# Optimization experiments

Hardware: AMD Instinct MI355X
Metric: run time of the kernel (lower is better)

The kernel has to match this reference:

```python
import jax, jax.numpy as jnp
import numpy as np

EPS = 1e-6

def _rmsnorm(x, w):
    # x: [..., Dh]
    inv = jax.lax.rsqrt(jnp.mean(x * x, axis=-1, keepdims=True) + EPS)
    return x * inv * w

def _apply_rope(x, rope):
    # x: [B, H, L, Dh], rope: [L, Dh//2, 2]
    L = x.shape[-2]
    cos = rope[:L, :, 0]  # [L, Dh//2]
    sin = rope[:L, :, 1]
    x_even = x[..., 0::2]
    x_odd = x[..., 1::2]
    rot = jnp.stack([x_even * cos - x_odd * sin,
                     x_even * sin + x_odd * cos], axis=-1)  # [B,H,L,Dh//2,2]
    return rot.reshape(*x.shape[:-1], -1)


def setup_inputs() -> dict:
    key = jax.random.key(0)
    ks = jax.random.split(key, 4)
    B, L, D = 2, 2048, 1024
    H, Dh = 16, 64
    x = jax.random.normal(ks[0], (B, L, D), dtype=jnp.float32)
    rope = jax.random.normal(ks[1], (L, Dh // 2, 2), dtype=jnp.float32)
    w_qkv = jax.random.normal(ks[2], (3 * D, D), dtype=jnp.float32) * (1.0 / np.sqrt(D))
    w_proj = jax.random.normal(ks[3], (D, D), dtype=jnp.float32) * (1.0 / np.sqrt(D))
    q_norm_w = jnp.ones((Dh,), dtype=jnp.float32)
    k_norm_w = jnp.ones((Dh,), dtype=jnp.float32)
    return {"x": x, "rope": rope, "w_qkv": w_qkv, "w_proj": w_proj,
            "q_norm_w": q_norm_w, "k_norm_w": k_norm_w}


def reference(x, rope, w_qkv, w_proj, q_norm_w, k_norm_w):
    B, L, D = x.shape
    H = 16
    Dh = D // H
    qkv = jnp.einsum('bld,ed->ble', x, w_qkv).reshape(B, L, 3, H, Dh)
    qkv = jnp.transpose(qkv, (2, 0, 3, 1, 4))  # [3, B, H, L, Dh]
    q, k, v = qkv[0], qkv[1], qkv[2]
    q = _rmsnorm(q, q_norm_w)
    k = _rmsnorm(k, k_norm_w)
    q = _apply_rope(q, rope)
    k = _apply_rope(k, rope)
    scale = 1.0 / np.sqrt(Dh)
    scores = jnp.einsum('bhqd,bhkd->bhqk', q, k) * scale
    attn = jax.nn.softmax(scores, axis=-1)
    out = jnp.einsum('bhqk,bhkd->bhqd', attn, v)  # [B,H,L,Dh]
    out = jnp.transpose(out, (0, 2, 1, 3)).reshape(B, L, D)
    return jnp.einsum('bld,ed->ble', out, w_proj)
```

## Files before the change

kernel.cpp:

```cpp
#include <hip/hip_runtime.h>

typedef unsigned short u16;
typedef unsigned int u32;
typedef __bf16 bf16x8 __attribute__((ext_vector_type(8)));
typedef float f32x4 __attribute__((ext_vector_type(4)));

#define L_SEQ 2048
#define NH 16
#define DH 64
#define D_MODEL 1024
#define ATT_SHIFT2 14.426950408889634f

__device__ __forceinline__ u16 f2bf(float f) {
  union { float f; u32 u; } v; v.f = f;
  u32 u = v.u;
  return (u16)((u + 0x7fffu + ((u >> 16) & 1u)) >> 16);
}
__device__ __forceinline__ float bf2f(u16 b) {
  union { u32 u; float f; } v; v.u = ((u32)b) << 16;
  return v.f;
}
__device__ __forceinline__ u32 pk2(float lo_val, float hi_val) {
  union { float f; u32 u; } a, b;
  a.f = hi_val; b.f = lo_val;
  return __builtin_amdgcn_perm(a.u + 0x8000u, b.u + 0x8000u, 0x07060302u);
}
__device__ __forceinline__ bf16x8 ld8(const u16* p) {
  union { uint4 u; bf16x8 b; } v;
  v.u = *(const uint4*)p;
  return v.b;
}
__device__ __forceinline__ f32x4 fzero4() { f32x4 z = {0.f, 0.f, 0.f, 0.f}; return z; }

__device__ __forceinline__ float fexp2(float x) {
#if __has_builtin(__builtin_amdgcn_exp2f)
  return __builtin_amdgcn_exp2f(x);
#else
  return __expf(x * 0.6931471805599453f);
#endif
}

__device__ __forceinline__ void gll16(const u16* g, u16* l) {
  __builtin_amdgcn_global_load_lds((const __attribute__((address_space(1))) u32*)g,
                                   (__attribute__((address_space(3))) u32*)l, 16, 0, 0);
}

__global__ __launch_bounds__(256) void cvt_bf16(const float* __restrict__ src,
                                                u16* __restrict__ dst, int n4) {
  int i = blockIdx.x * 256 + threadIdx.x;
  if (i >= n4) return;
  float4 v = ((const float4*)src)[i];
  ushort4 o = make_ushort4(f2bf(v.x), f2bf(v.y), f2bf(v.z), f2bf(v.w));
  ((ushort4*)dst)[i] = o;
}

template <int BM, bool OUT_BF16>
__global__ __launch_bounds__(256) void gemm_bt(const u16* __restrict__ A,
                                               const u16* __restrict__ B,
                                               void* __restrict__ Cp,
                                               int N, int K) {
  constexpr int MI = BM / 32;
  __shared__ u16 As[BM * 64];
  __shared__ u16 Bs[128 * 64];
  const int t = threadIdx.x;
  const int lane = t & 63, wv = t >> 6;
  const int col = lane & 15, quad = lane >> 4;
  const int wr = wv >> 1, wc = wv & 1;
  const int m0 = blockIdx.y * BM, n0 = blockIdx.x * 128;

  f32x4 acc[MI][4];
#pragma unroll
  for (int i = 0; i < MI; ++i)
#pragma unroll
    for (int j = 0; j < 4; ++j) acc[i][j] = fzero4();

  for (int kt = 0; kt < K; kt += 64) {
    __syncthreads();
#pragma unroll
    for (int it = 0; it < BM / 32; ++it) {
      int id0 = it * 256 + wv * 64;
      int id = id0 + lane;
      int row = id >> 3, cs = id & 7;
      int csrc = cs ^ (row & 7);
      gll16(A + (size_t)(m0 + row) * K + kt + csrc * 8, As + (size_t)id0 * 8);
    }
#pragma unroll
    for (int it = 0; it < 4; ++it) {
      int id0 = it * 256 + wv * 64;
      int id = id0 + lane;
      int row = id >> 3, cs = id & 7;
      int csrc = cs ^ (row & 7);
      gll16(B + (size_t)(n0 + row) * K + kt + csrc * 8, Bs + (size_t)id0 * 8);
    }
    __syncthreads();
#pragma unroll
    for (int c = 0; c < 2; ++c) {
      bf16x8 af[MI], bfv[4];
#pragma unroll
      for (int f = 0; f < MI; ++f) {
        int r = wr * (BM / 2) + f * 16 + col;
        af[f] = ld8(&As[(r * 8 + ((c * 4 + quad) ^ (r & 7))) * 8]);
      }
#pragma unroll
      for (int f = 0; f < 4; ++f) {
        int rb = wc * 64 + f * 16 + col;
        bfv[f] = ld8(&Bs[(rb * 8 + ((c * 4 + quad) ^ (rb & 7))) * 8]);
      }
#pragma unroll
      for (int i = 0; i < MI; ++i)
#pragma unroll
        for (int j = 0; j < 4; ++j)
          acc[i][j] = __builtin_amdgcn_mfma_f32_16x16x32_bf16(af[i], bfv[j], acc[i][j], 0, 0, 0);
    }
  }
#pragma unroll
  for (int i = 0; i < MI; ++i) {
    int gr = m0 + wr * (BM / 2) + i * 16 + quad * 4;
#pragma unroll
    for (int j = 0; j < 4; ++j) {
      int gc = n0 + wc * 64 + j * 16 + col;
#pragma unroll
      for (int r = 0; r < 4; ++r) {
        if (OUT_BF16)
          ((u16*)Cp)[(size_t)(gr + r) * N + gc] = f2bf(acc[i][j][r]);
        else
          ((float*)Cp)[(size_t)(gr + r) * N + gc] = acc[i][j][r];
      }
    }
  }
}

__global__ __launch_bounds__(256) void qk_norm_rope(const u16* __restrict__ qkvb,
                                                    const float* __restrict__ rope,
                                                    const float* __restrict__ qw,
                                                    const float* __restrict__ kw,
                                                    u16* __restrict__ qb,
                                                    u16* __restrict__ kb) {
  const int t = threadIdx.x;
  const int lane = t & 63, wv = t >> 6;
  const int gid = blockIdx.x * 4 + wv;
  const int l = gid & (L_SEQ - 1);
  const int b = gid >> 11;
  const int lg = lane & 7;
  const u16* base = qkvb + (size_t)gid * 3072 + lane * 8;
  const float QSCALE = 0.125f * 1.4426950408889634f;

  float wqv[8], wkv[8], rp[8];
  {
    float4 a = *(const float4*)(qw + lg * 8);
    float4 c = *(const float4*)(qw + lg * 8 + 4);
    wqv[0]=a.x; wqv[1]=a.y; wqv[2]=a.z; wqv[3]=a.w; wqv[4]=c.x; wqv[5]=c.y; wqv[6]=c.z; wqv[7]=c.w;
    a = *(const float4*)(kw + lg * 8);
    c = *(const float4*)(kw + lg * 8 + 4);
    wkv[0]=a.x; wkv[1]=a.y; wkv[2]=a.z; wkv[3]=a.w; wkv[4]=c.x; wkv[5]=c.y; wkv[6]=c.z; wkv[7]=c.w;
    a = *(const float4*)(rope + (size_t)l * 64 + lg * 8);
    c = *(const float4*)(rope + (size_t)l * 64 + lg * 8 + 4);
    rp[0]=a.x; rp[1]=a.y; rp[2]=a.z; rp[3]=a.w; rp[4]=c.x; rp[5]=c.y; rp[6]=c.z; rp[7]=c.w;
  }

#pragma unroll
  for (int i = 0; i < 2; ++i) {
    bf16x8 q8 = ld8(base + i * 512);
    bf16x8 k8 = ld8(base + 1024 + i * 512);
    float q[8], k[8];
#pragma unroll
    for (int j = 0; j < 8; ++j) { q[j] = (float)q8[j]; k[j] = (float)k8[j]; }
    float sq = 0.f, sk = 0.f;
#pragma unroll
    for (int j = 0; j < 8; ++j) { sq += q[j] * q[j]; sk += k[j] * k[j]; }
    sq += __shfl_xor(sq, 1); sq += __shfl_xor(sq, 2); sq += __shfl_xor(sq, 4);
    sk += __shfl_xor(sk, 1); sk += __shfl_xor(sk, 2); sk += __shfl_xor(sk, 4);
    float qi = rsqrtf(sq * (1.f / 64.f) + 1e-6f);
    float ki = rsqrtf(sk * (1.f / 64.f) + 1e-6f);

    float rq[8], rk[8];
#pragma unroll
    for (int j = 0; j < 4; ++j) {
      float cs = rp[2 * j], sn = rp[2 * j + 1];
      float qe = q[2 * j] * qi * wqv[2 * j], qo = q[2 * j + 1] * qi * wqv[2 * j + 1];
      float ke = k[2 * j] * ki * wkv[2 * j], ko = k[2 * j + 1] * ki * wkv[2 * j + 1];
      rq[2 * j]     = (qe * cs - qo * sn) * QSCALE;
      rq[2 * j + 1] = (qe * sn + qo * cs) * QSCALE;
      rk[2 * j]     = ke * cs - ko * sn;
      rk[2 * j + 1] = ke * sn + ko * cs;
    }
    uint4 qp = make_uint4(pk2(rq[0], rq[1]), pk2(rq[2], rq[3]), pk2(rq[4], rq[5]), pk2(rq[6], rq[7]));
    uint4 kp = make_uint4(pk2(rk[0], rk[1]), pk2(rk[2], rk[3]), pk2(rk[4], rk[5]), pk2(rk[6], rk[7]));
    const int head = (lane >> 3) + i * 8;
    size_t oi = (((size_t)(b * NH + head) * L_SEQ + l) * DH) + lg * 8;
    *(uint4*)(qb + oi) = qp;
    *(uint4*)(kb + oi) = kp;
  }
}

__global__ __launch_bounds__(256) void v_transpose(const u16* __restrict__ qkvb,
                                                   u16* __restrict__ vtb) {
  __shared__ u16 ldsT[64 * 64];
  const int t = threadIdx.x;
  const int bid = blockIdx.x;
  const int bh = bid >> 5;
  const int lt = (bid & 31) * 64;
  const int b = bh >> 4, h = bh & 15;
  const u16* src = qkvb + (size_t)(b * L_SEQ + lt) * 3072 + 2048 + h * 64;
#pragma unroll
  for (int i = 0; i < 2; ++i) {
    int idx = i * 256 + t;
    int ll = idx >> 3, dc = idx & 7;
    uint4 v = *(const uint4*)(src + (size_t)ll * 3072 + dc * 8);
    union { uint4 u; u16 s[8]; } vv; vv.u = v;
#pragma unroll
    for (int j = 0; j < 8; ++j) {
      int dh = dc * 8 + j;
      ldsT[dh * 64 + ((((ll >> 3) ^ (dh >> 3)) & 7) * 8 + (ll & 7))] = vv.s[j];
    }
  }
  __syncthreads();
#pragma unroll
  for (int i = 0; i < 2; ++i) {
    int idx = i * 256 + t;
    int dh = idx >> 3, lc = idx & 7;
    uint4 v = *(const uint4*)&ldsT[dh * 64 + (((lc ^ (dh >> 3)) & 7) * 8)];
    *(uint4*)(vtb + ((size_t)bh * 64 + dh) * L_SEQ + lt + lc * 8) = v;
  }
}

__global__ __launch_bounds__(256) void attn_flash(const u16* __restrict__ qb,
                                                  const u16* __restrict__ kb,
                                                  const u16* __restrict__ vtb,
                                                  u16* __restrict__ po,
                                                  float* __restrict__ pl) {
  __shared__ u16 ldsK[2 * 4096];
  __shared__ u16 ldsV[2 * 4096];
  __shared__ u16 ldsP[4 * 32 * 72];
  const int t = threadIdx.x;
  const int lane = t & 63, wv = t >> 6;
  const int col = lane & 15, quad = lane >> 4;
  const int bh = blockIdx.x;
  const int q0 = blockIdx.y * 128 + wv * 32;
  const int half = blockIdx.z;

  const u16* kbase = kb + ((size_t)bh * L_SEQ + half * 1024) * DH;
  const u16* vbase = vtb + (size_t)bh * DH * L_SEQ + half * 1024;

  bf16x8 qfrag[2][2];
#pragma unroll
  for (int qf = 0; qf < 2; ++qf)
#pragma unroll
    for (int c = 0; c < 2; ++c)
      qfrag[qf][c] = ld8(qb + ((size_t)bh * L_SEQ + q0 + qf * 16 + col) * DH + c * 32 + quad * 8);

  f32x4 o[2][4];
#pragma unroll
  for (int qf = 0; qf < 2; ++qf)
#pragma unroll
    for (int nf = 0; nf < 4; ++nf) o[qf][nf] = fzero4();
  float lrow[2] = {0.f, 0.f};

#pragma unroll
  for (int it = 0; it < 2; ++it) {
    int id0 = it * 256 + wv * 64;
    int id = id0 + lane;
    int row = id >> 3, cs = id & 7, csrc = cs ^ (row & 7);
    gll16(kbase + row * DH + csrc * 8, ldsK + (size_t)id0 * 8);
    gll16(vbase + (size_t)row * L_SEQ + csrc * 8, ldsV + (size_t)id0 * 8);
  }

  u16* pb = &ldsP[wv * 32 * 72];

  for (int tt = 0; tt < 16; ++tt) {
    __syncthreads();
    const int cur = (tt & 1) * 4096;
    if (tt + 1 < 16) {
      const int nxt = ((tt + 1) & 1) * 4096;
      const int kt = (tt + 1) * 64;
#pragma unroll
      for (int it = 0; it < 2; ++it) {
        int id0 = it * 256 + wv * 64;
        int id = id0 + lane;
        int row = id >> 3, cs = id & 7, csrc = cs ^ (row & 7);
        gll16(kbase + (size_t)(kt + row) * DH + csrc * 8, ldsK + nxt + (size_t)id0 * 8);
        gll16(vbase + (size_t)row * L_SEQ + kt + csrc * 8, ldsV + nxt + (size_t)id0 * 8);
      }
    }

    f32x4 s[2][4];
#pragma unroll
    for (int qf = 0; qf < 2; ++qf)
#pragma unroll
      for (int mf = 0; mf < 4; ++mf) s[qf][mf] = fzero4();
#pragma unroll
    for (int c = 0; c < 2; ++c) {
#pragma unroll
      for (int mf = 0; mf < 4; ++mf) {
        int kr = mf * 16 + col;
        bf16x8 kf = ld8(&ldsK[cur + kr * 64 + (((c * 4 + quad) ^ (kr & 7)) * 8)]);
#pragma unroll
        for (int qf = 0; qf < 2; ++qf)
          s[qf][mf] = __builtin_amdgcn_mfma_f32_16x16x32_bf16(kf, qfrag[qf][c], s[qf][mf], 0, 0, 0);
      }
    }

#pragma unroll
    for (int qf = 0; qf < 2; ++qf) {
      float ts = 0.f;
#pragma unroll
      for (int mf = 0; mf < 4; ++mf)
#pragma unroll
        for (int r = 0; r < 4; ++r) {
          float e = fexp2(s[qf][mf][r] - ATT_SHIFT2);
          s[qf][mf][r] = e;
          ts += e;
        }
      lrow[qf] += ts;
      u16* prow = pb + (qf * 16 + col) * 72;
#pragma unroll
      for (int mf = 0; mf < 4; ++mf) {
        u32 lo = pk2(s[qf][mf][0], s[qf][mf][1]);
        u32 hi = pk2(s[qf][mf][2], s[qf][mf][3]);
        *(uint2*)(prow + ((mf ^ (col & 3)) * 16 + quad * 4)) = make_uint2(lo, hi);
      }
    }

#pragma unroll
    for (int c = 0; c < 2; ++c) {
      bf16x8 pa[2];
#pragma unroll
      for (int qf = 0; qf < 2; ++qf)
        pa[qf] = ld8(pb + (qf * 16 + col) * 72 +
                     (((c * 2 + (quad >> 1)) ^ (col & 3)) * 16 + (quad & 1) * 8));
#pragma unroll
      for (int nf = 0; nf < 4; ++nf) {
        int vr = nf * 16 + col;
        bf16x8 vf = ld8(&ldsV[cur + vr * 64 + (((c * 4 + quad) ^ (vr & 7)) * 8)]);
#pragma unroll
        for (int qf = 0; qf < 2; ++qf)
          o[qf][nf] = __builtin_amdgcn_mfma_f32_16x16x32_bf16(pa[qf], vf, o[qf][nf], 0, 0, 0);
      }
    }
  }

  u16* pob = po + (size_t)(half * 32 + bh) * L_SEQ * DH;
#pragma unroll
  for (int qf = 0; qf < 2; ++qf) {
    lrow[qf] += __shfl_xor(lrow[qf], 16);
    lrow[qf] += __shfl_xor(lrow[qf], 32);
    if (quad == 0)
      pl[(size_t)(half * 32 + bh) * L_SEQ + q0 + qf * 16 + col] = lrow[qf];
#pragma unroll
    for (int nf = 0; nf < 4; ++nf)
#pragma unroll
      for (int r = 0; r < 4; ++r)
        pob[(size_t)(q0 + qf * 16 + quad * 4 + r) * DH + nf * 16 + col] = f2bf(o[qf][nf][r]);
  }
}

__global__ __launch_bounds__(256) void attn_combine(const u16* __restrict__ po,
                                                    const float* __restrict__ pl,
                                                    u16* __restrict__ ob) {
  int j = blockIdx.x * 256 + threadIdx.x;
  int bh = j >> 14;
  int rem = j & 16383;
  int l = rem >> 3, dc = rem & 7;
  size_t pidx = ((size_t)bh * L_SEQ + l) * DH + dc * 8;
  uint4 a = *(const uint4*)(po + pidx);
  uint4 c = *(const uint4*)(po + 4194304 + pidx);
  float inv = 1.f / (pl[(size_t)bh * L_SEQ + l] + pl[65536 + (size_t)bh * L_SEQ + l]);
  union { uint4 u; u16 s[8]; } ua, uc; ua.u = a; uc.u = c;
  float r[8];
#pragma unroll
  for (int i = 0; i < 8; ++i) r[i] = (bf2f(ua.s[i]) + bf2f(uc.s[i])) * inv;
  uint4 out = make_uint4(pk2(r[0], r[1]), pk2(r[2], r[3]), pk2(r[4], r[5]), pk2(r[6], r[7]));
  int b = bh >> 4, h = bh & 15;
  *(uint4*)(ob + ((size_t)(b * L_SEQ + l)) * D_MODEL + h * 64 + dc * 8) = out;
}

extern "C" void kernel_launch(void* const* d_in, const int* in_sizes, int n_in,
                              void* d_out, int out_size, void* d_ws, size_t ws_size,
                              hipStream_t stream) {
  const float* x     = (const float*)d_in[0];
  const float* rope  = (const float*)d_in[1];
  const float* wqkv  = (const float*)d_in[2];
  const float* wproj = (const float*)d_in[3];
  const float* qnw   = (const float*)d_in[4];
  const float* knw   = (const float*)d_in[5];
  float* out = (float*)d_out;
  char* ws = (char*)d_ws;

  u16* xb     = (u16*)(ws + 0);
  u16* wqkvb  = (u16*)(ws + 8388608);
  u16* wprojb = (u16*)(ws + 14680064);
  u16* qkvb   = (u16*)(ws + 16777216);
  u16* qb     = (u16*)(ws + 41943040);
  u16* kb     = (u16*)(ws + 50331648);
  u16* vtb    = (u16*)(ws + 58720256);
  u16* ob     = xb;
  u16* po     = qkvb;
  float* pl   = (float*)(ws + 33554432);

  cvt_bf16<<<4096, 256, 0, stream>>>(x, xb, 1048576);
  cvt_bf16<<<3072, 256, 0, stream>>>(wqkv, wqkvb, 786432);
  cvt_bf16<<<1024, 256, 0, stream>>>(wproj, wprojb, 262144);

  gemm_bt<128, true><<<dim3(24, 32), 256, 0, stream>>>(xb, wqkvb, (void*)qkvb, 3072, 1024);

  qk_norm_rope<<<1024, 256, 0, stream>>>(qkvb, rope, qnw, knw, qb, kb);
  v_transpose<<<1024, 256, 0, stream>>>(qkvb, vtb);

  attn_flash<<<dim3(32, 16, 2), 256, 0, stream>>>(qb, kb, vtb, po, pl);
  attn_combine<<<2048, 256, 0, stream>>>(po, pl, ob);

  gemm_bt<64, false><<<dim3(8, 64), 256, 0, stream>>>(ob, wprojb, (void*)out, 1024, 1024);
}
```

Measured before the change: 210.0 us.

## Fuse attention split-combine into output projection GEMM and restructure P staging

The separate attn_combine kernel is removed. The output projection GEMM now reads both split-K partial outputs and their row sums directly, normalizes them and converts to bf16 while staging the A tile in LDS. This saves one kernel launch and a full round trip of the combined output through memory. The attention kernel also packs P per query-fragment into a smaller, XOR-swizzled LDS buffer using truncating bf16 packing, and places the two halves of a head in adjacent blocks. The new GEMM does not overlap its loads (no double buffering), and each A tile is loaded twice from global memory and recomputed in every column block.

```diff
diff --git a/kernel.cpp b/kernel.cpp
--- a/kernel.cpp
+++ b/kernel.cpp
@@ -24,6 +24,11 @@
   union { float f; u32 u; } a, b;
   a.f = hi_val; b.f = lo_val;
   return __builtin_amdgcn_perm(a.u + 0x8000u, b.u + 0x8000u, 0x07060302u);
+}
+__device__ __forceinline__ u32 pk2t(float lo_val, float hi_val) {
+  union { float f; u32 u; } a, b;
+  a.f = hi_val; b.f = lo_val;
+  return __builtin_amdgcn_perm(a.u, b.u, 0x07060302u);
 }
 __device__ __forceinline__ bf16x8 ld8(const u16* p) {
   union { uint4 u; bf16x8 b; } v;
@@ -231,13 +236,13 @@
                                                   float* __restrict__ pl) {
   __shared__ u16 ldsK[2 * 4096];
   __shared__ u16 ldsV[2 * 4096];
-  __shared__ u16 ldsP[4 * 32 * 72];
+  __shared__ u16 ldsP[4 * 1024];
   const int t = threadIdx.x;
   const int lane = t & 63, wv = t >> 6;
   const int col = lane & 15, quad = lane >> 4;
-  const int bh = blockIdx.x;
+  const int bh = blockIdx.x >> 1;
+  const int half = blockIdx.x & 1;
   const int q0 = blockIdx.y * 128 + wv * 32;
-  const int half = blockIdx.z;
 
   const u16* kbase = kb + ((size_t)bh * L_SEQ + half * 1024) * DH;
   const u16* vbase = vtb + (size_t)bh * DH * L_SEQ + half * 1024;
@@ -265,7 +270,7 @@
     gll16(vbase + (size_t)row * L_SEQ + csrc * 8, ldsV + (size_t)id0 * 8);
   }
 
-  u16* pb = &ldsP[wv * 32 * 72];
+  u16* pb = &ldsP[wv * 1024];
 
   for (int tt = 0; tt < 16; ++tt) {
     __syncthreads();
@@ -312,29 +317,21 @@
           ts += e;
         }
       lrow[qf] += ts;
-      u16* prow = pb + (qf * 16 + col) * 72;
 #pragma unroll
       for (int mf = 0; mf < 4; ++mf) {
-        u32 lo = pk2(s[qf][mf][0], s[qf][mf][1]);
-        u32 hi = pk2(s[qf][mf][2], s[qf][mf][3]);
-        *(uint2*)(prow + ((mf ^ (col & 3)) * 16 + quad * 4)) = make_uint2(lo, hi);
-      }
-    }
-
-#pragma unroll
-    for (int c = 0; c < 2; ++c) {
-      bf16x8 pa[2];
-#pragma unroll
-      for (int qf = 0; qf < 2; ++qf)
-        pa[qf] = ld8(pb + (qf * 16 + col) * 72 +
-                     (((c * 2 + (quad >> 1)) ^ (col & 3)) * 16 + (quad & 1) * 8));
-#pragma unroll
-      for (int nf = 0; nf < 4; ++nf) {
-        int vr = nf * 16 + col;
-        bf16x8 vf = ld8(&ldsV[cur + vr * 64 + (((c * 4 + quad) ^ (vr & 7)) * 8)]);
-#pragma unroll
-        for (int qf = 0; qf < 2; ++qf)
-          o[qf][nf] = __builtin_amdgcn_mfma_f32_16x16x32_bf16(pa[qf], vf, o[qf][nf], 0, 0, 0);
+        int slot = col * 8 + (((2 * mf + (quad >> 1))) ^ (col & 7));
+        *(uint2*)(pb + slot * 8 + (quad & 1) * 4) =
+            make_uint2(pk2t(s[qf][mf][0], s[qf][mf][1]), pk2t(s[qf][mf][2], s[qf][mf][3]));
+      }
+#pragma unroll
+      for (int c = 0; c < 2; ++c) {
+        bf16x8 pa = ld8(pb + (col * 8 + ((c * 4 + quad) ^ (col & 7))) * 8);
+#pragma unroll
+        for (int nf = 0; nf < 4; ++nf) {
+          int vr = nf * 16 + col;
+          bf16x8 vf = ld8(&ldsV[cur + vr * 64 + (((c * 4 + quad) ^ (vr & 7)) * 8)]);
+          o[qf][nf] = __builtin_amdgcn_mfma_f32_16x16x32_bf16(pa, vf, o[qf][nf], 0, 0, 0);
+        }
       }
     }
   }
@@ -354,24 +351,87 @@
   }
 }
 
-__global__ __launch_bounds__(256) void attn_combine(const u16* __restrict__ po,
-                                                    const float* __restrict__ pl,
-                                                    u16* __restrict__ ob) {
-  int j = blockIdx.x * 256 + threadIdx.x;
-  int bh = j >> 14;
-  int rem = j & 16383;
-  int l = rem >> 3, dc = rem & 7;
-  size_t pidx = ((size_t)bh * L_SEQ + l) * DH + dc * 8;
-  uint4 a = *(const uint4*)(po + pidx);
-  uint4 c = *(const uint4*)(po + 4194304 + pidx);
-  float inv = 1.f / (pl[(size_t)bh * L_SEQ + l] + pl[65536 + (size_t)bh * L_SEQ + l]);
-  union { uint4 u; u16 s[8]; } ua, uc; ua.u = a; uc.u = c;
-  float r[8];
-#pragma unroll
-  for (int i = 0; i < 8; ++i) r[i] = (bf2f(ua.s[i]) + bf2f(uc.s[i])) * inv;
-  uint4 out = make_uint4(pk2(r[0], r[1]), pk2(r[2], r[3]), pk2(r[4], r[5]), pk2(r[6], r[7]));
-  int b = bh >> 4, h = bh & 15;
-  *(uint4*)(ob + ((size_t)(b * L_SEQ + l)) * D_MODEL + h * 64 + dc * 8) = out;
+__global__ __launch_bounds__(256) void gemm2_cmb(const u16* __restrict__ po,
+                                                 const float* __restrict__ pl,
+                                                 const u16* __restrict__ B,
+                                                 float* __restrict__ out) {
+  __shared__ u16 As[64 * 64];
+  __shared__ u16 Bs[128 * 64];
+  const int t = threadIdx.x;
+  const int lane = t & 63, wv = t >> 6;
+  const int col = lane & 15, quad = lane >> 4;
+  const int wr = wv >> 1, wc = wv & 1;
+  const int m0 = blockIdx.y * 64, n0 = blockIdx.x * 128;
+  const int srow = t >> 2, kc0 = (t & 3) * 2;
+  const int m = m0 + srow, bb = m >> 11, ll = m & 2047;
+
+  f32x4 acc[2][4];
+#pragma unroll
+  for (int i = 0; i < 2; ++i)
+#pragma unroll
+    for (int j = 0; j < 4; ++j) acc[i][j] = fzero4();
+
+  for (int kt = 0; kt < 1024; kt += 64) {
+    __syncthreads();
+    {
+      int h = kt >> 6;
+      size_t lidx = (size_t)(bb * 16 + h) * L_SEQ + ll;
+      float inv = 1.0f / (pl[lidx] + pl[65536 + lidx]);
+      size_t rowoff = lidx * 64;
+#pragma unroll
+      for (int i = 0; i < 2; ++i) {
+        int kc = kc0 + i;
+        uint4 a0 = *(const uint4*)(po + rowoff + kc * 8);
+        uint4 a1 = *(const uint4*)(po + 4194304 + rowoff + kc * 8);
+        union { uint4 u; u16 s[8]; } ua, ub;
+        ua.u = a0; ub.u = a1;
+        float r[8];
+#pragma unroll
+        for (int j = 0; j < 8; ++j) r[j] = (bf2f(ua.s[j]) + bf2f(ub.s[j])) * inv;
+        uint4 pk = make_uint4(pk2(r[0], r[1]), pk2(r[2], r[3]), pk2(r[4], r[5]), pk2(r[6], r[7]));
+        int slot = srow * 8 + (kc ^ (srow & 7));
+        *(uint4*)(As + slot * 8) = pk;
+      }
+    }
+#pragma unroll
+    for (int it = 0; it < 4; ++it) {
+      int id0 = it * 256 + wv * 64;
+      int id = id0 + lane;
+      int row = id >> 3, cs = id & 7, csrc = cs ^ (row & 7);
+      gll16(B + (size_t)(n0 + row) * 1024 + kt + csrc * 8, Bs + (size_t)id0 * 8);
+    }
+    __syncthreads();
+#pragma unroll
+    for (int c = 0; c < 2; ++c) {
+      bf16x8 af[2], bfv[4];
+#pragma unroll
+      for (int f = 0; f < 2; ++f) {
+        int r = wr * 32 + f * 16 + col;
+        af[f] = ld8(&As[(r * 8 + ((c * 4 + quad) ^ (r & 7))) * 8]);
+      }
+#pragma unroll
+      for (int f = 0; f < 4; ++f) {
+        int rb = wc * 64 + f * 16 + col;
+        bfv[f] = ld8(&Bs[(rb * 8 + ((c * 4 + quad) ^ (rb & 7))) * 8]);
+      }
+#pragma unroll
+      for (int i = 0; i < 2; ++i)
+#pragma unroll
+        for (int j = 0; j < 4; ++j)
+          acc[i][j] = __builtin_amdgcn_mfma_f32_16x16x32_bf16(af[i], bfv[j], acc[i][j], 0, 0, 0);
+    }
+  }
+#pragma unroll
+  for (int i = 0; i < 2; ++i) {
+    int gr = m0 + wr * 32 + i * 16 + quad * 4;
+#pragma unroll
+    for (int j = 0; j < 4; ++j) {
+      int gc = n0 + wc * 64 + j * 16 + col;
+#pragma unroll
+      for (int r = 0; r < 4; ++r)
+        out[(size_t)(gr + r) * D_MODEL + gc] = acc[i][j][r];
+    }
+  }
 }
 
 extern "C" void kernel_launch(void* const* d_in, const int* in_sizes, int n_in,
@@ -393,7 +453,6 @@
   u16* qb     = (u16*)(ws + 41943040);
   u16* kb     = (u16*)(ws + 50331648);
   u16* vtb    = (u16*)(ws + 58720256);
-  u16* ob     = xb;
   u16* po     = qkvb;
   float* pl   = (float*)(ws + 33554432);
 
@@ -406,8 +465,7 @@
   qk_norm_rope<<<1024, 256, 0, stream>>>(qkvb, rope, qnw, knw, qb, kb);
   v_transpose<<<1024, 256, 0, stream>>>(qkvb, vtb);
 
-  attn_flash<<<dim3(32, 16, 2), 256, 0, stream>>>(qb, kb, vtb, po, pl);
-  attn_combine<<<2048, 256, 0, stream>>>(po, pl, ob);
-
-  gemm_bt<64, false><<<dim3(8, 64), 256, 0, stream>>>(ob, wprojb, (void*)out, 1024, 1024);
-}
+  attn_flash<<<dim3(64, 16), 256, 0, stream>>>(qb, kb, vtb, po, pl);
+
+  gemm2_cmb<<<dim3(8, 64), 256, 0, stream>>>(po, pl, wprojb, out);
+}
```

After: 212.4 us. Within noise of the previous version (+1.1%).
